# Kernel optimization log

Hardware: AMD Instinct MI355X
Metric: run time of the kernel (lower is better)

## Reference

```python
import jax, jax.numpy as jnp
import numpy as np

N, E, D_IN, D_H, G = 50000, 800000, 300, 128, 128


def gat_conv(x, src, dst, W, att_src, att_dst, bias):
    # PyG GATConv, heads=1, concat, negative_slope=0.2, self-loops already appended.
    h = x @ W                              # [N, F]
    a_s = h @ att_src                      # [N]
    a_d = h @ att_dst                      # [N]
    e = jax.nn.leaky_relu(a_s[src] + a_d[dst], 0.2)   # [E+N]
    m = jax.ops.segment_max(e, dst, num_segments=h.shape[0])
    ex = jnp.exp(e - m[dst])
    denom = jax.ops.segment_sum(ex, dst, num_segments=h.shape[0])
    alpha = ex / denom[dst]                # softmax over in-edges of each dst
    out = jax.ops.segment_sum(alpha[:, None] * h[src], dst, num_segments=h.shape[0])
    return out + bias


def setup_inputs() -> dict:
    key = jax.random.key(0)
    ks = jax.random.split(key, 12)
    x = jax.random.normal(ks[0], (N, D_IN), dtype=jnp.float32)
    edge_index = jax.random.randint(ks[1], (2, E), 0, N)
    batch = jnp.sort(jax.random.randint(ks[2], (N,), 0, G))
    pos = jax.random.randint(ks[3], (N,), 0, 2).astype(bool)
    s = 0.05
    W1 = jax.random.normal(ks[4], (D_IN, D_H), dtype=jnp.float32) * s
    as1 = jax.random.normal(ks[5], (D_H,), dtype=jnp.float32) * s
    ad1 = jax.random.normal(ks[6], (D_H,), dtype=jnp.float32) * s
    b1 = jnp.zeros((D_H,), dtype=jnp.float32)
    W2 = jax.random.normal(ks[7], (D_H, D_H), dtype=jnp.float32) * s
    as2 = jax.random.normal(ks[8], (D_H,), dtype=jnp.float32) * s
    ad2 = jax.random.normal(ks[9], (D_H,), dtype=jnp.float32) * s
    b2 = jnp.zeros((D_H,), dtype=jnp.float32)
    Wfc = jax.random.normal(ks[10], (D_H, 1), dtype=jnp.float32) * s
    bfc = jnp.zeros((1,), dtype=jnp.float32)
    return {"x": x, "edge_index": edge_index, "batch": batch, "pos": pos,
            "num_graphs": G, "W1": W1, "as1": as1, "ad1": ad1, "b1": b1,
            "W2": W2, "as2": as2, "ad2": ad2, "b2": b2, "Wfc": Wfc, "bfc": bfc}


def reference(x, edge_index, batch, pos, num_graphs, W1, as1, ad1, b1,
              W2, as2, ad2, b2, Wfc, bfc):
    n = x.shape[0]
    loop = jnp.arange(n)
    src = jnp.concatenate([edge_index[0], loop])
    dst = jnp.concatenate([edge_index[1], loop])
    h = gat_conv(x, src, dst, W1, as1, ad1, b1)
    h = jax.nn.gelu(h, approximate=False)
    # dropout is identity in eval mode
    h = gat_conv(h, src, dst, W2, as2, ad2, b2)   # [N, 128]
    # masked per-graph mean: logits[g] = mean over nodes with batch==g and pos
    w = pos.astype(h.dtype)                       # [N]
    sums = jax.ops.segment_sum(h * w[:, None], batch, num_segments=num_graphs)
    cnt = jax.ops.segment_sum(w, batch, num_segments=num_graphs)
    logits = sums / jnp.maximum(cnt, 1.0)[:, None]          # [G, 128]
    scores = (jax.nn.gelu(logits, approximate=False) @ Wfc + bfc).reshape(-1, num_graphs)
    return scores, logits
```

## Files before the change

kernel.cpp:

```cpp
#include <hip/hip_runtime.h>
#include <math.h>

#define NN 50000
#define EE 800000
#define DIN 300
#define DH 128
#define NG 128
#define LDA 40
#define RSIZE 6250

typedef __attribute__((ext_vector_type(8))) short short8;
typedef __attribute__((ext_vector_type(4))) float floatx4;

__device__ __forceinline__ float gelu_exact(float x) {
  return 0.5f * x * (1.0f + erff(x * 0.7071067811865476f));
}

__device__ __forceinline__ void split_bf16(float v, unsigned short& hi, unsigned short& lo) {
  unsigned int u = __float_as_uint(v);
  hi = (unsigned short)(u >> 16);
  float fh = __uint_as_float((unsigned int)hi << 16);
  lo = (unsigned short)(__float_as_uint(v - fh) >> 16);
}

__device__ __forceinline__ unsigned short f2bf_rne(float x) {
  unsigned int u = __float_as_uint(x);
  unsigned int r = (u + 0x7FFFu + ((u >> 16) & 1u)) >> 16;
  return (unsigned short)r;
}

__device__ __forceinline__ float bf_lo(unsigned u) { return __uint_as_float(u << 16); }
__device__ __forceinline__ float bf_hi(unsigned u) { return __uint_as_float(u & 0xFFFF0000u); }


__global__ __launch_bounds__(256) void count_part_kernel(const int* __restrict__ ei,
                                                         int* __restrict__ deg,
                                                         int blocksPerRange) {
  const int r = blockIdx.x & 7;
  const int t = blockIdx.x >> 3;
  const int lo = r * RSIZE, hi = lo + RSIZE;
  const int total = EE + NN;
  const int step = blocksPerRange * 256;
  for (int e0 = t * 256; e0 < total; e0 += step) {
    int e = e0 + threadIdx.x;
    if (e < total) {
      int d = (e < EE) ? ei[EE + e] : (e - EE);
      if (d >= lo && d < hi) atomicAdd(&deg[d], 1);
    }
  }
}

__global__ __launch_bounds__(1024) void scan_part_kernel(const int* __restrict__ deg,
                                                         int* __restrict__ rowptr,
                                                         int* __restrict__ bsum) {
  __shared__ int wsum[16];
  const int tid = threadIdx.x;
  const int lane = tid & 63;
  const int wid = tid >> 6;
  int idx = blockIdx.x * 1024 + tid;
  int v = (idx < NN) ? deg[idx] : 0;
  int x = v;
#pragma unroll
  for (int d = 1; d < 64; d <<= 1) {
    int y = __shfl_up(x, d, 64);
    if (lane >= d) x += y;
  }
  if (lane == 63) wsum[wid] = x;
  __syncthreads();
  if (wid == 0) {
    int s = (lane < 16) ? wsum[lane] : 0;
#pragma unroll
    for (int d = 1; d < 16; d <<= 1) {
      int y = __shfl_up(s, d, 64);
      if (lane >= d) s += y;
    }
    if (lane < 16) wsum[lane] = s;
  }
  __syncthreads();
  int woff = (wid > 0) ? wsum[wid - 1] : 0;
  int incl = x + woff;
  if (idx < NN) rowptr[idx] = incl - v;
  if (tid == 1023) bsum[blockIdx.x] = incl;
}

__global__ __launch_bounds__(64) void scan_sums_kernel(const int* __restrict__ bsum,
                                                       int* __restrict__ boff, int nb) {
  int lane = threadIdx.x;
  int v = (lane < nb) ? bsum[lane] : 0;
  int x = v;
#pragma unroll
  for (int d = 1; d < 64; d <<= 1) {
    int y = __shfl_up(x, d, 64);
    if (lane >= d) x += y;
  }
  if (lane < nb) boff[lane] = x - v;
  if (lane == nb - 1) boff[nb] = x;
}

__global__ __launch_bounds__(256) void scan_add_kernel(int* __restrict__ rowptr,
                                                       const int* __restrict__ boff,
                                                       int* __restrict__ cursor, int nb) {
  int i = blockIdx.x * 256 + threadIdx.x;
  if (i < NN) {
    int r = rowptr[i] + boff[i >> 10];
    rowptr[i] = r;
    cursor[i] = r;
  } else if (i == NN) {
    rowptr[NN] = boff[nb];
  }
}

__global__ __launch_bounds__(256) void scatter_part_kernel(const int* __restrict__ ei,
                                                           int* __restrict__ cursor,
                                                           int* __restrict__ colA,
                                                           int blocksPerRange) {
  const int r = blockIdx.x & 7;
  const int t = blockIdx.x >> 3;
  const int lo = r * RSIZE, hi = lo + RSIZE;
  const int total = EE + NN;
  const int step = blocksPerRange * 256;
  for (int e0 = t * 256; e0 < total; e0 += step) {
    int e = e0 + threadIdx.x;
    if (e < total) {
      int d = (e < EE) ? ei[EE + e] : (e - EE);
      if (d >= lo && d < hi) {
        int s = (e < EE) ? ei[e] : d;
        int p = atomicAdd(&cursor[d], 1);
        colA[p] = s;
      }
    }
  }
}


__global__ __launch_bounds__(256) void convert_bt_kernel(const float* __restrict__ B,
                                                         unsigned short* __restrict__ Bth,
                                                         unsigned short* __restrict__ Btl,
                                                         int K, int Kpad) {
  int i = blockIdx.x * 256 + threadIdx.x;
  int n = i / Kpad, k = i % Kpad;
  if (n >= 128) return;
  float v = (k < K) ? B[(long)k * 128 + n] : 0.f;
  unsigned short h, l;
  split_bf16(v, h, l);
  Bth[(long)n * Kpad + k] = h;
  Btl[(long)n * Kpad + k] = l;
}


__global__ __launch_bounds__(256) void gemm_mfma_kernel(
    const float* __restrict__ A,
    const unsigned short* __restrict__ Bth, const unsigned short* __restrict__ Btl,
    unsigned short* __restrict__ C, int M, int K, int Kpad,
    const float* __restrict__ avs, const float* __restrict__ avd,
    float* __restrict__ aS, float* __restrict__ aD) {
  __shared__ unsigned short Ah[64 * LDA];
  __shared__ unsigned short Al[64 * LDA];
  __shared__ unsigned short Bh[128 * LDA];
  __shared__ unsigned short Bl[128 * LDA];

  const int tid = threadIdx.x;
  const int lane = tid & 63;
  const int w = tid >> 6;
  const int wr = w >> 1, wc = w & 1;
  const int q = lane >> 4;
  const int m16 = lane & 15;
  const int row0 = blockIdx.x * 64;

  floatx4 acc[2][4];
#pragma unroll
  for (int i = 0; i < 2; i++)
#pragma unroll
    for (int j = 0; j < 4; j++) acc[i][j] = (floatx4)(0.f);

  const int nsteps = Kpad / 32;
  for (int s = 0; s < nsteps; s++) {
    const int k0 = s * 32;
#pragma unroll
    for (int p = 0; p < 2; p++) {
      int e = p * 256 + tid;
      int r = e >> 3;
      int q4 = e & 7;
      int gr = row0 + r, gk = k0 + q4 * 4;
      float4 v = make_float4(0.f, 0.f, 0.f, 0.f);
      if (gr < M && gk < K) v = *(const float4*)&A[(long)gr * K + gk];
      unsigned short h0, h1, h2, h3, l0, l1, l2, l3;
      split_bf16(v.x, h0, l0);
      split_bf16(v.y, h1, l1);
      split_bf16(v.z, h2, l2);
      split_bf16(v.w, h3, l3);
      uint2 hh, ll;
      hh.x = (unsigned)h0 | ((unsigned)h1 << 16);
      hh.y = (unsigned)h2 | ((unsigned)h3 << 16);
      ll.x = (unsigned)l0 | ((unsigned)l1 << 16);
      ll.y = (unsigned)l2 | ((unsigned)l3 << 16);
      *(uint2*)&Ah[r * LDA + q4 * 4] = hh;
      *(uint2*)&Al[r * LDA + q4 * 4] = ll;
    }
#pragma unroll
    for (int p = 0; p < 2; p++) {
      int e = p * 256 + tid;
      int n = e & 127;
      int sel = e >> 7;
      const unsigned short* src = (sel & 2) ? Btl : Bth;
      unsigned short* dst = (sel & 2) ? Bl : Bh;
      int kk = (sel & 1) * 16;
      uint4 v0 = *(const uint4*)&src[(long)n * Kpad + k0 + kk];
      uint4 v1 = *(const uint4*)&src[(long)n * Kpad + k0 + kk + 8];
      *(uint4*)&dst[n * LDA + kk] = v0;
      *(uint4*)&dst[n * LDA + kk + 8] = v1;
    }
    __syncthreads();
    short8 afh[2], afl[2];
#pragma unroll
    for (int rt = 0; rt < 2; rt++) {
      int r = wr * 32 + rt * 16 + m16;
      afh[rt] = *(const short8*)&Ah[r * LDA + q * 8];
      afl[rt] = *(const short8*)&Al[r * LDA + q * 8];
    }
#pragma unroll
    for (int ct = 0; ct < 4; ct++) {
      int n = wc * 64 + ct * 16 + m16;
      short8 bfh = *(const short8*)&Bh[n * LDA + q * 8];
      short8 bfl = *(const short8*)&Bl[n * LDA + q * 8];
#pragma unroll
      for (int rt = 0; rt < 2; rt++) {
        acc[rt][ct] = __builtin_amdgcn_mfma_f32_16x16x32_bf16(afh[rt], bfh, acc[rt][ct], 0, 0, 0);
        acc[rt][ct] = __builtin_amdgcn_mfma_f32_16x16x32_bf16(afh[rt], bfl, acc[rt][ct], 0, 0, 0);
        acc[rt][ct] = __builtin_amdgcn_mfma_f32_16x16x32_bf16(afl[rt], bfh, acc[rt][ct], 0, 0, 0);
      }
    }
    __syncthreads();
  }

  float avs_r[4], avd_r[4];
#pragma unroll
  for (int ct = 0; ct < 4; ct++) {
    int n = wc * 64 + ct * 16 + m16;
    avs_r[ct] = avs[n];
    avd_r[ct] = avd[n];
  }
#pragma unroll
  for (int rt = 0; rt < 2; rt++) {
    int rbase = row0 + wr * 32 + rt * 16 + q * 4;
#pragma unroll
    for (int reg = 0; reg < 4; reg++) {
      int grow = rbase + reg;
      bool ok = grow < M;
      float ps = 0.f, pd = 0.f;
#pragma unroll
      for (int ct = 0; ct < 4; ct++) {
        float c = acc[rt][ct][reg];
        if (ok) C[(long)grow * 128 + wc * 64 + ct * 16 + m16] = f2bf_rne(c);
        ps = fmaf(c, avs_r[ct], ps);
        pd = fmaf(c, avd_r[ct], pd);
      }
#pragma unroll
      for (int d = 1; d < 16; d <<= 1) {
        ps += __shfl_xor(ps, d, 64);
        pd += __shfl_xor(pd, d, 64);
      }
      if (m16 == 0 && ok) {
        atomicAdd(&aS[grow], ps);
        atomicAdd(&aD[grow], pd);
      }
    }
  }
}


__global__ __launch_bounds__(256) void aggregate_kernel(const int* __restrict__ rowptr,
                                                        const int* __restrict__ colA,
                                                        const float* __restrict__ aS,
                                                        const float* __restrict__ aD,
                                                        const unsigned short* __restrict__ Hb,
                                                        const float* __restrict__ bias,
                                                        float* __restrict__ out,
                                                        int apply_gelu) {
  const int lane = threadIdx.x & 63;
  const int dst = blockIdx.x * 4 + (threadIdx.x >> 6);
  if (dst >= NN) return;
  const int start = rowptr[dst];
  const int end = rowptr[dst + 1];
  const int deg = end - start;
  const float ad = aD[dst];
  const int half = lane >> 5;
  const int fl = lane & 31;

  float a0 = 0.f, a1 = 0.f, a2 = 0.f, a3 = 0.f;

  if (deg <= 64) {
    int src = 0;
    float e = -__builtin_inff();
    if (lane < deg) {
      src = colA[start + lane];
      float v = aS[src] + ad;
      e = (v > 0.f) ? v : 0.2f * v;
    }
    float mx = e;
#pragma unroll
    for (int d = 1; d < 64; d <<= 1) mx = fmaxf(mx, __shfl_xor(mx, d, 64));
    float ew = (lane < deg) ? expf(e - mx) : 0.f;
    float ss = ew;
#pragma unroll
    for (int d = 1; d < 64; d <<= 1) ss += __shfl_xor(ss, d, 64);
    float wgt = ew * (1.f / ss);
    for (int j = 0; j < deg; j += 4) {
      int j0 = j + half;
      int j1 = j + 2 + half;
      int sj0 = __shfl(src, j0, 64);
      float wj0 = __shfl(wgt, j0, 64);
      int sj1 = __shfl(src, j1, 64);
      float wj1 = __shfl(wgt, j1, 64);
      uint2 u0 = *(const uint2*)&Hb[(long)sj0 * DH + fl * 4];
      uint2 u1 = *(const uint2*)&Hb[(long)sj1 * DH + fl * 4];
      a0 = fmaf(wj0, bf_lo(u0.x), a0);
      a1 = fmaf(wj0, bf_hi(u0.x), a1);
      a2 = fmaf(wj0, bf_lo(u0.y), a2);
      a3 = fmaf(wj0, bf_hi(u0.y), a3);
      a0 = fmaf(wj1, bf_lo(u1.x), a0);
      a1 = fmaf(wj1, bf_hi(u1.x), a1);
      a2 = fmaf(wj1, bf_lo(u1.y), a2);
      a3 = fmaf(wj1, bf_hi(u1.y), a3);
    }
  } else {
    float m = -__builtin_inff(), ssum = 0.f;
    for (int c0 = start; c0 < end; c0 += 64) {
      int i = c0 + lane;
      float e = -__builtin_inff();
      if (i < end) {
        int s = colA[i];
        float v = aS[s] + ad;
        e = (v > 0.f) ? v : 0.2f * v;
      }
      float cm = e;
#pragma unroll
      for (int d = 1; d < 64; d <<= 1) cm = fmaxf(cm, __shfl_xor(cm, d, 64));
      float ce = (i < end) ? expf(e - cm) : 0.f;
      float cs = ce;
#pragma unroll
      for (int d = 1; d < 64; d <<= 1) cs += __shfl_xor(cs, d, 64);
      float nm = fmaxf(m, cm);
      ssum = ssum * expf(m - nm) + cs * expf(cm - nm);
      m = nm;
    }
    float inv = 1.f / ssum;
    for (int c0 = start; c0 < end; c0 += 64) {
      int i = c0 + lane;
      int src = 0;
      float wgt = 0.f;
      if (i < end) {
        src = colA[i];
        float v = aS[src] + ad;
        float e = (v > 0.f) ? v : 0.2f * v;
        wgt = expf(e - m) * inv;
      }
      int lim = min(64, end - c0);
      for (int j = 0; j < lim; j += 4) {
        int j0 = j + half;
        int j1 = j + 2 + half;
        int sj0 = __shfl(src, j0, 64);
        float wj0 = __shfl(wgt, j0, 64);
        int sj1 = __shfl(src, j1, 64);
        float wj1 = __shfl(wgt, j1, 64);
        uint2 u0 = *(const uint2*)&Hb[(long)sj0 * DH + fl * 4];
        uint2 u1 = *(const uint2*)&Hb[(long)sj1 * DH + fl * 4];
        a0 = fmaf(wj0, bf_lo(u0.x), a0);
        a1 = fmaf(wj0, bf_hi(u0.x), a1);
        a2 = fmaf(wj0, bf_lo(u0.y), a2);
        a3 = fmaf(wj0, bf_hi(u0.y), a3);
        a0 = fmaf(wj1, bf_lo(u1.x), a0);
        a1 = fmaf(wj1, bf_hi(u1.x), a1);
        a2 = fmaf(wj1, bf_lo(u1.y), a2);
        a3 = fmaf(wj1, bf_hi(u1.y), a3);
      }
    }
  }

  a0 += __shfl_xor(a0, 32, 64);
  a1 += __shfl_xor(a1, 32, 64);
  a2 += __shfl_xor(a2, 32, 64);
  a3 += __shfl_xor(a3, 32, 64);

  if (half == 0) {
    float4 b = *(const float4*)&bias[fl * 4];
    float r0 = a0 + b.x;
    float r1 = a1 + b.y;
    float r2 = a2 + b.z;
    float r3 = a3 + b.w;
    if (apply_gelu) {
      r0 = gelu_exact(r0); r1 = gelu_exact(r1);
      r2 = gelu_exact(r2); r3 = gelu_exact(r3);
    }
    *(float4*)&out[(long)dst * DH + fl * 4] = make_float4(r0, r1, r2, r3);
  }
}


__global__ __launch_bounds__(128) void pool_kernel(const float* __restrict__ H,
                                                   const int* __restrict__ batch,
                                                   const int* __restrict__ pos,
                                                   float* __restrict__ sums,
                                                   float* __restrict__ cnt) {
  const int CH = 64;
  int n0 = blockIdx.x * CH;
  int n1 = min(n0 + CH, NN);
  int f = threadIdx.x;
  float acc = 0.f, c = 0.f;
  int g = batch[n0];
  for (int n = n0; n < n1; n++) {
    int gn = batch[n];
    if (gn != g) {
      atomicAdd(&sums[g * DH + f], acc);
      if (f == 0) atomicAdd(&cnt[g], c);
      acc = 0.f; c = 0.f; g = gn;
    }
    if (pos[n]) {
      acc += H[(long)n * DH + f];
      c += 1.f;
    }
  }
  atomicAdd(&sums[g * DH + f], acc);
  if (f == 0) atomicAdd(&cnt[g], c);
}


__global__ __launch_bounds__(128) void head_kernel(const float* __restrict__ sums,
                                                   const float* __restrict__ cnt,
                                                   const float* __restrict__ Wfc,
                                                   const float* __restrict__ bfc,
                                                   float* __restrict__ out) {
  int g = blockIdx.x;
  int f = threadIdx.x;
  float c = fmaxf(cnt[g], 1.f);
  float logit = sums[g * DH + f] / c;
  out[NG + g * DH + f] = logit;
  float gl = gelu_exact(logit) * Wfc[f];
  __shared__ float red[2];
#pragma unroll
  for (int d = 1; d < 64; d <<= 1) gl += __shfl_xor(gl, d, 64);
  int lane = f & 63, w = f >> 6;
  if (lane == 0) red[w] = gl;
  __syncthreads();
  if (f == 0) out[g] = red[0] + red[1] + bfc[0];
}


extern "C" void kernel_launch(void* const* d_in, const int* in_sizes, int n_in,
                              void* d_out, int out_size, void* d_ws, size_t ws_size,
                              hipStream_t stream) {
  const float* x   = (const float*)d_in[0];
  const int* ei    = (const int*)d_in[1];
  const int* batch = (const int*)d_in[2];
  const int* pos   = (const int*)d_in[3];
  const float* W1  = (const float*)d_in[5];
  const float* as1 = (const float*)d_in[6];
  const float* ad1 = (const float*)d_in[7];
  const float* b1  = (const float*)d_in[8];
  const float* W2  = (const float*)d_in[9];
  const float* as2 = (const float*)d_in[10];
  const float* ad2 = (const float*)d_in[11];
  const float* b2  = (const float*)d_in[12];
  const float* Wfc = (const float*)d_in[13];
  const float* bfc = (const float*)d_in[14];
  float* out = (float*)d_out;

  const int KP1 = 320;
  const int KP2 = 128;
  const int NB_SCAN = (NN + 1023) / 1024;
  const int BPR = 416;

  char* ws = (char*)d_ws;
  size_t off = 0;
  auto nxt = [&](size_t b) -> void* {
    size_t p = off;
    off += (b + 255) & ~(size_t)255;
    return (void*)(ws + p);
  };
  int* rowptr = (int*)nxt((NN + 1) * sizeof(int));
  int* cursor = (int*)nxt(NN * sizeof(int));
  int* colA   = (int*)nxt((size_t)(EE + NN) * sizeof(int));
  int* bsum   = (int*)nxt((NB_SCAN + 1) * sizeof(int));
  int* boff   = (int*)nxt((NB_SCAN + 1) * sizeof(int));
  float* aS   = (float*)nxt((size_t)2 * NN * sizeof(float));
  float* aD   = aS + NN;
  unsigned short* bufAb = (unsigned short*)nxt((size_t)NN * DH * sizeof(short));
  float* bufB = (float*)nxt((size_t)NN * DH * sizeof(float));
  float* sums = (float*)nxt((size_t)(NG * DH + NG) * sizeof(float));
  float* cnt  = sums + NG * DH;
  unsigned short* Bt1h = (unsigned short*)nxt((size_t)128 * KP1 * sizeof(short));
  unsigned short* Bt1l = (unsigned short*)nxt((size_t)128 * KP1 * sizeof(short));
  unsigned short* Bt2h = (unsigned short*)nxt((size_t)128 * KP2 * sizeof(short));
  unsigned short* Bt2l = (unsigned short*)nxt((size_t)128 * KP2 * sizeof(short));

  hipMemsetAsync(cursor, 0, NN * sizeof(int), stream);
  hipMemsetAsync(sums, 0, (NG * DH + NG) * sizeof(float), stream);
  hipMemsetAsync(aS, 0, (size_t)2 * NN * sizeof(float), stream);

  convert_bt_kernel<<<(128 * KP1 + 255) / 256, 256, 0, stream>>>(W1, Bt1h, Bt1l, DIN, KP1);
  convert_bt_kernel<<<(128 * KP2 + 255) / 256, 256, 0, stream>>>(W2, Bt2h, Bt2l, DH, KP2);

  count_part_kernel<<<8 * BPR, 256, 0, stream>>>(ei, cursor, BPR);
  scan_part_kernel<<<NB_SCAN, 1024, 0, stream>>>(cursor, rowptr, bsum);
  scan_sums_kernel<<<1, 64, 0, stream>>>(bsum, boff, NB_SCAN);
  scan_add_kernel<<<(NN + 1 + 255) / 256, 256, 0, stream>>>(rowptr, boff, cursor, NB_SCAN);
  scatter_part_kernel<<<8 * BPR, 256, 0, stream>>>(ei, cursor, colA, BPR);

  const int gblocks = (NN + 63) / 64;
  gemm_mfma_kernel<<<gblocks, 256, 0, stream>>>(x, Bt1h, Bt1l, bufAb, NN, DIN, KP1,
                                                as1, ad1, aS, aD);
  aggregate_kernel<<<(NN + 3) / 4, 256, 0, stream>>>(rowptr, colA, aS, aD, bufAb, b1, bufB, 1);
  hipMemsetAsync(aS, 0, (size_t)2 * NN * sizeof(float), stream);
  gemm_mfma_kernel<<<gblocks, 256, 0, stream>>>(bufB, Bt2h, Bt2l, bufAb, NN, DH, KP2,
                                                as2, ad2, aS, aD);
  aggregate_kernel<<<(NN + 3) / 4, 256, 0, stream>>>(rowptr, colA, aS, aD, bufAb, b2, bufB, 0);
  pool_kernel<<<(NN + 63) / 64, 128, 0, stream>>>(bufB, batch, pos, sums, cnt);
  head_kernel<<<NG, 128, 0, stream>>>(sums, cnt, Wfc, bfc, out);
}
```

Measured before the change: 366.4 us.

## Prefetch next K-tile into registers during MFMA compute in split-bf16 GEMM

```diff
diff --git a/kernel.cpp b/kernel.cpp
--- a/kernel.cpp
+++ b/kernel.cpp
@@ -167,6 +167,11 @@
   const int m16 = lane & 15;
   const int row0 = blockIdx.x * 64;
 
+  const int ar = tid >> 3;
+  const int aq4 = tid & 7;
+  const int bn = tid & 127;
+  const int bkk = (tid >> 7) * 16;
+
   floatx4 acc[2][4];
 #pragma unroll
   for (int i = 0; i < 2; i++)
@@ -174,43 +179,61 @@
     for (int j = 0; j < 4; j++) acc[i][j] = (floatx4)(0.f);
 
   const int nsteps = Kpad / 32;
+
+  float4 vA0, vA1;
+  uint4 vB00, vB01, vB10, vB11;
+
+  auto issue_loads = [&](int s) {
+    const int k0 = s * 32;
+    const int gk = k0 + aq4 * 4;
+    int gr0 = row0 + ar;
+    vA0 = make_float4(0.f, 0.f, 0.f, 0.f);
+    vA1 = make_float4(0.f, 0.f, 0.f, 0.f);
+    if (gk < K) {
+      if (gr0 < M) vA0 = *(const float4*)&A[(long)gr0 * K + gk];
+      if (gr0 + 32 < M) vA1 = *(const float4*)&A[(long)(gr0 + 32) * K + gk];
+    }
+    const long bb = (long)bn * Kpad + k0 + bkk;
+    vB00 = *(const uint4*)&Bth[bb];
+    vB01 = *(const uint4*)&Bth[bb + 8];
+    vB10 = *(const uint4*)&Btl[bb];
+    vB11 = *(const uint4*)&Btl[bb + 8];
+  };
+
+  auto write_stage = [&]() {
+    unsigned short h0, h1, h2, h3, l0, l1, l2, l3;
+    split_bf16(vA0.x, h0, l0);
+    split_bf16(vA0.y, h1, l1);
+    split_bf16(vA0.z, h2, l2);
+    split_bf16(vA0.w, h3, l3);
+    uint2 hh, ll;
+    hh.x = (unsigned)h0 | ((unsigned)h1 << 16);
+    hh.y = (unsigned)h2 | ((unsigned)h3 << 16);
+    ll.x = (unsigned)l0 | ((unsigned)l1 << 16);
+    ll.y = (unsigned)l2 | ((unsigned)l3 << 16);
+    *(uint2*)&Ah[ar * LDA + aq4 * 4] = hh;
+    *(uint2*)&Al[ar * LDA + aq4 * 4] = ll;
+    split_bf16(vA1.x, h0, l0);
+    split_bf16(vA1.y, h1, l1);
+    split_bf16(vA1.z, h2, l2);
+    split_bf16(vA1.w, h3, l3);
+    hh.x = (unsigned)h0 | ((unsigned)h1 << 16);
+    hh.y = (unsigned)h2 | ((unsigned)h3 << 16);
+    ll.x = (unsigned)l0 | ((unsigned)l1 << 16);
+    ll.y = (unsigned)l2 | ((unsigned)l3 << 16);
+    *(uint2*)&Ah[(ar + 32) * LDA + aq4 * 4] = hh;
+    *(uint2*)&Al[(ar + 32) * LDA + aq4 * 4] = ll;
+    *(uint4*)&Bh[bn * LDA + bkk] = vB00;
+    *(uint4*)&Bh[bn * LDA + bkk + 8] = vB01;
+    *(uint4*)&Bl[bn * LDA + bkk] = vB10;
+    *(uint4*)&Bl[bn * LDA + bkk + 8] = vB11;
+  };
+
+  issue_loads(0);
   for (int s = 0; s < nsteps; s++) {
-    const int k0 = s * 32;
-#pragma unroll
-    for (int p = 0; p < 2; p++) {
-      int e = p * 256 + tid;
-      int r = e >> 3;
-      int q4 = e & 7;
-      int gr = row0 + r, gk = k0 + q4 * 4;
-      float4 v = make_float4(0.f, 0.f, 0.f, 0.f);
-      if (gr < M && gk < K) v = *(const float4*)&A[(long)gr * K + gk];
-      unsigned short h0, h1, h2, h3, l0, l1, l2, l3;
-      split_bf16(v.x, h0, l0);
-      split_bf16(v.y, h1, l1);
-      split_bf16(v.z, h2, l2);
-      split_bf16(v.w, h3, l3);
-      uint2 hh, ll;
-      hh.x = (unsigned)h0 | ((unsigned)h1 << 16);
-      hh.y = (unsigned)h2 | ((unsigned)h3 << 16);
-      ll.x = (unsigned)l0 | ((unsigned)l1 << 16);
-      ll.y = (unsigned)l2 | ((unsigned)l3 << 16);
-      *(uint2*)&Ah[r * LDA + q4 * 4] = hh;
-      *(uint2*)&Al[r * LDA + q4 * 4] = ll;
-    }
-#pragma unroll
-    for (int p = 0; p < 2; p++) {
-      int e = p * 256 + tid;
-      int n = e & 127;
-      int sel = e >> 7;
-      const unsigned short* src = (sel & 2) ? Btl : Bth;
-      unsigned short* dst = (sel & 2) ? Bl : Bh;
-      int kk = (sel & 1) * 16;
-      uint4 v0 = *(const uint4*)&src[(long)n * Kpad + k0 + kk];
-      uint4 v1 = *(const uint4*)&src[(long)n * Kpad + k0 + kk + 8];
-      *(uint4*)&dst[n * LDA + kk] = v0;
-      *(uint4*)&dst[n * LDA + kk + 8] = v1;
-    }
+    write_stage();
     __syncthreads();
+    if (s + 1 < nsteps) issue_loads(s + 1);
     short8 afh[2], afl[2];
 #pragma unroll
     for (int rt = 0; rt < 2; rt++) {
```

After: 364.7 us. Within noise of the previous version (-0.5%).

## Restructure GEMM: register-resident A fragments, async double-buffered B, drop atomics

Applied to the files above, without the earlier changes.

```diff
diff --git a/kernel.cpp b/kernel.cpp
--- a/kernel.cpp
+++ b/kernel.cpp
@@ -6,7 +6,6 @@
 #define DIN 300
 #define DH 128
 #define NG 128
-#define LDA 40
 #define RSIZE 6250
 
 typedef __attribute__((ext_vector_type(8))) short short8;
@@ -31,6 +30,13 @@
 
 __device__ __forceinline__ float bf_lo(unsigned u) { return __uint_as_float(u << 16); }
 __device__ __forceinline__ float bf_hi(unsigned u) { return __uint_as_float(u & 0xFFFF0000u); }
+
+__device__ __forceinline__ void async_ld16(void* lds, const void* g) {
+  __builtin_amdgcn_global_load_lds(
+      (const __attribute__((address_space(1))) unsigned int*)(unsigned long long)g,
+      (__attribute__((address_space(3))) unsigned int*)(unsigned int)(unsigned long long)lds,
+      16, 0, 0);
+}
 
 
 __global__ __launch_bounds__(256) void count_part_kernel(const int* __restrict__ ei,
@@ -154,116 +160,115 @@
     unsigned short* __restrict__ C, int M, int K, int Kpad,
     const float* __restrict__ avs, const float* __restrict__ avd,
     float* __restrict__ aS, float* __restrict__ aD) {
-  __shared__ unsigned short Ah[64 * LDA];
-  __shared__ unsigned short Al[64 * LDA];
-  __shared__ unsigned short Bh[128 * LDA];
-  __shared__ unsigned short Bl[128 * LDA];
+  __shared__ __align__(16) unsigned short Bls[2][2][128 * 32];
 
   const int tid = threadIdx.x;
   const int lane = tid & 63;
   const int w = tid >> 6;
-  const int wr = w >> 1, wc = w & 1;
   const int q = lane >> 4;
   const int m16 = lane & 15;
   const int row0 = blockIdx.x * 64;
-
-  floatx4 acc[2][4];
-#pragma unroll
-  for (int i = 0; i < 2; i++)
-#pragma unroll
-    for (int j = 0; j < 4; j++) acc[i][j] = (floatx4)(0.f);
+  const int myrow = row0 + w * 16 + m16;
+  const bool rok = myrow < M;
+  const long abase = (long)myrow * K;
+
+  const int rl = lane >> 2, qq0 = lane & 3;
+  const int nb0 = w * 16 + rl;
+  const int nb1 = 64 + w * 16 + rl;
+  const long boff0 = (long)nb0 * Kpad + (long)((qq0 ^ ((nb0 >> 1) & 3)) * 8);
+  const long boff1 = (long)nb1 * Kpad + (long)((qq0 ^ ((nb1 >> 1) & 3)) * 8);
+
+  floatx4 acc[8];
+#pragma unroll
+  for (int i = 0; i < 8; i++) acc[i] = (floatx4)(0.f);
 
   const int nsteps = Kpad / 32;
+
+  float4 vA0, vA1, nA0, nA1;
+  nA0 = nA1 = make_float4(0.f, 0.f, 0.f, 0.f);
+
+  auto stageB = [&](int s, int nb) {
+    const int k0 = s * 32;
+    async_ld16(&Bls[nb][0][(w * 16) * 32], Bth + boff0 + k0);
+    async_ld16(&Bls[nb][0][(64 + w * 16) * 32], Bth + boff1 + k0);
+    async_ld16(&Bls[nb][1][(w * 16) * 32], Btl + boff0 + k0);
+    async_ld16(&Bls[nb][1][(64 + w * 16) * 32], Btl + boff1 + k0);
+  };
+  auto loadA = [&](int s, float4& x0, float4& x1) {
+    const int k0 = s * 32 + q * 8;
+    x0 = make_float4(0.f, 0.f, 0.f, 0.f);
+    x1 = x0;
+    if (rok) {
+      if (k0 + 4 <= K) x0 = *(const float4*)&A[abase + k0];
+      if (k0 + 8 <= K) x1 = *(const float4*)&A[abase + k0 + 4];
+    }
+  };
+
+  stageB(0, 0);
+  loadA(0, vA0, vA1);
+  __syncthreads();
+
   for (int s = 0; s < nsteps; s++) {
-    const int k0 = s * 32;
-#pragma unroll
-    for (int p = 0; p < 2; p++) {
-      int e = p * 256 + tid;
-      int r = e >> 3;
-      int q4 = e & 7;
-      int gr = row0 + r, gk = k0 + q4 * 4;
-      float4 v = make_float4(0.f, 0.f, 0.f, 0.f);
-      if (gr < M && gk < K) v = *(const float4*)&A[(long)gr * K + gk];
-      unsigned short h0, h1, h2, h3, l0, l1, l2, l3;
-      split_bf16(v.x, h0, l0);
-      split_bf16(v.y, h1, l1);
-      split_bf16(v.z, h2, l2);
-      split_bf16(v.w, h3, l3);
-      uint2 hh, ll;
-      hh.x = (unsigned)h0 | ((unsigned)h1 << 16);
-      hh.y = (unsigned)h2 | ((unsigned)h3 << 16);
-      ll.x = (unsigned)l0 | ((unsigned)l1 << 16);
-      ll.y = (unsigned)l2 | ((unsigned)l3 << 16);
-      *(uint2*)&Ah[r * LDA + q4 * 4] = hh;
-      *(uint2*)&Al[r * LDA + q4 * 4] = ll;
-    }
-#pragma unroll
-    for (int p = 0; p < 2; p++) {
-      int e = p * 256 + tid;
-      int n = e & 127;
-      int sel = e >> 7;
-      const unsigned short* src = (sel & 2) ? Btl : Bth;
-      unsigned short* dst = (sel & 2) ? Bl : Bh;
-      int kk = (sel & 1) * 16;
-      uint4 v0 = *(const uint4*)&src[(long)n * Kpad + k0 + kk];
-      uint4 v1 = *(const uint4*)&src[(long)n * Kpad + k0 + kk + 8];
-      *(uint4*)&dst[n * LDA + kk] = v0;
-      *(uint4*)&dst[n * LDA + kk + 8] = v1;
-    }
+    const int cur = s & 1;
+    if (s + 1 < nsteps) {
+      stageB(s + 1, 1 ^ cur);
+      loadA(s + 1, nA0, nA1);
+    }
+    float av[8] = {vA0.x, vA0.y, vA0.z, vA0.w, vA1.x, vA1.y, vA1.z, vA1.w};
+    union {
+      unsigned u[4];
+      short8 s8;
+    } Uh, Ul;
+#pragma unroll
+    for (int i = 0; i < 4; i++) {
+      unsigned short ha, la, hb, lb;
+      split_bf16(av[2 * i], ha, la);
+      split_bf16(av[2 * i + 1], hb, lb);
+      Uh.u[i] = (unsigned)ha | ((unsigned)hb << 16);
+      Ul.u[i] = (unsigned)la | ((unsigned)lb << 16);
+    }
+    short8 afh = Uh.s8, afl = Ul.s8;
+#pragma unroll
+    for (int ct = 0; ct < 8; ct++) {
+      int n = ct * 16 + m16;
+      int qv = (q ^ ((n >> 1) & 3)) * 8;
+      short8 bfh = *(const short8*)&Bls[cur][0][n * 32 + qv];
+      short8 bfl = *(const short8*)&Bls[cur][1][n * 32 + qv];
+      acc[ct] = __builtin_amdgcn_mfma_f32_16x16x32_bf16(afh, bfh, acc[ct], 0, 0, 0);
+      acc[ct] = __builtin_amdgcn_mfma_f32_16x16x32_bf16(afh, bfl, acc[ct], 0, 0, 0);
+      acc[ct] = __builtin_amdgcn_mfma_f32_16x16x32_bf16(afl, bfh, acc[ct], 0, 0, 0);
+    }
+    vA0 = nA0;
+    vA1 = nA1;
     __syncthreads();
-    short8 afh[2], afl[2];
-#pragma unroll
-    for (int rt = 0; rt < 2; rt++) {
-      int r = wr * 32 + rt * 16 + m16;
-      afh[rt] = *(const short8*)&Ah[r * LDA + q * 8];
-      afl[rt] = *(const short8*)&Al[r * LDA + q * 8];
-    }
-#pragma unroll
-    for (int ct = 0; ct < 4; ct++) {
-      int n = wc * 64 + ct * 16 + m16;
-      short8 bfh = *(const short8*)&Bh[n * LDA + q * 8];
-      short8 bfl = *(const short8*)&Bl[n * LDA + q * 8];
-#pragma unroll
-      for (int rt = 0; rt < 2; rt++) {
-        acc[rt][ct] = __builtin_amdgcn_mfma_f32_16x16x32_bf16(afh[rt], bfh, acc[rt][ct], 0, 0, 0);
-        acc[rt][ct] = __builtin_amdgcn_mfma_f32_16x16x32_bf16(afh[rt], bfl, acc[rt][ct], 0, 0, 0);
-        acc[rt][ct] = __builtin_amdgcn_mfma_f32_16x16x32_bf16(afl[rt], bfh, acc[rt][ct], 0, 0, 0);
-      }
-    }
-    __syncthreads();
-  }
-
-  float avs_r[4], avd_r[4];
-#pragma unroll
-  for (int ct = 0; ct < 4; ct++) {
-    int n = wc * 64 + ct * 16 + m16;
-    avs_r[ct] = avs[n];
-    avd_r[ct] = avd[n];
-  }
-#pragma unroll
-  for (int rt = 0; rt < 2; rt++) {
-    int rbase = row0 + wr * 32 + rt * 16 + q * 4;
-#pragma unroll
-    for (int reg = 0; reg < 4; reg++) {
-      int grow = rbase + reg;
-      bool ok = grow < M;
-      float ps = 0.f, pd = 0.f;
-#pragma unroll
-      for (int ct = 0; ct < 4; ct++) {
-        float c = acc[rt][ct][reg];
-        if (ok) C[(long)grow * 128 + wc * 64 + ct * 16 + m16] = f2bf_rne(c);
-        ps = fmaf(c, avs_r[ct], ps);
-        pd = fmaf(c, avd_r[ct], pd);
-      }
-#pragma unroll
-      for (int d = 1; d < 16; d <<= 1) {
-        ps += __shfl_xor(ps, d, 64);
-        pd += __shfl_xor(pd, d, 64);
-      }
-      if (m16 == 0 && ok) {
-        atomicAdd(&aS[grow], ps);
-        atomicAdd(&aD[grow], pd);
-      }
+  }
+
+  float avs_r[8], avd_r[8];
+#pragma unroll
+  for (int ct = 0; ct < 8; ct++) {
+    avs_r[ct] = avs[ct * 16 + m16];
+    avd_r[ct] = avd[ct * 16 + m16];
+  }
+#pragma unroll
+  for (int reg = 0; reg < 4; reg++) {
+    int grow = row0 + w * 16 + q * 4 + reg;
+    bool ok = grow < M;
+    float ps = 0.f, pd = 0.f;
+#pragma unroll
+    for (int ct = 0; ct < 8; ct++) {
+      float c = acc[ct][reg];
+      if (ok) C[(long)grow * 128 + ct * 16 + m16] = f2bf_rne(c);
+      ps = fmaf(c, avs_r[ct], ps);
+      pd = fmaf(c, avd_r[ct], pd);
+    }
+#pragma unroll
+    for (int d = 1; d < 16; d <<= 1) {
+      ps += __shfl_xor(ps, d, 64);
+      pd += __shfl_xor(pd, d, 64);
+    }
+    if (m16 == 0 && ok) {
+      aS[grow] = ps;
+      aD[grow] = pd;
     }
   }
 }
@@ -495,7 +500,6 @@
 
   hipMemsetAsync(cursor, 0, NN * sizeof(int), stream);
   hipMemsetAsync(sums, 0, (NG * DH + NG) * sizeof(float), stream);
-  hipMemsetAsync(aS, 0, (size_t)2 * NN * sizeof(float), stream);
 
   convert_bt_kernel<<<(128 * KP1 + 255) / 256, 256, 0, stream>>>(W1, Bt1h, Bt1l, DIN, KP1);
   convert_bt_kernel<<<(128 * KP2 + 255) / 256, 256, 0, stream>>>(W2, Bt2h, Bt2l, DH, KP2);
@@ -510,7 +514,6 @@
   gemm_mfma_kernel<<<gblocks, 256, 0, stream>>>(x, Bt1h, Bt1l, bufAb, NN, DIN, KP1,
                                                 as1, ad1, aS, aD);
   aggregate_kernel<<<(NN + 3) / 4, 256, 0, stream>>>(rowptr, colA, aS, aD, bufAb, b1, bufB, 1);
-  hipMemsetAsync(aS, 0, (size_t)2 * NN * sizeof(float), stream);
   gemm_mfma_kernel<<<gblocks, 256, 0, stream>>>(bufB, Bt2h, Bt2l, bufAb, NN, DH, KP2,
                                                 as2, ad2, aS, aD);
   aggregate_kernel<<<(NN + 3) / 4, 256, 0, stream>>>(rowptr, colA, aS, aD, bufAb, b2, bufB, 0);
```

Result: faster. 344.4 us (-6.0%).
